# Kernel optimization log

Measured on AMD Instinct MI355X. Metric: run time of the kernel, lower is better.

## Reference

```python
import jax, jax.numpy as jnp
import numpy as np
from jax import lax

B, CIN, COUT, K, SDIM, H = 8, 512, 512, 3, 512, 32
EPS = 1e-8
LRELU_SLOPE = 0.2
ACT_SCALE = float(np.sqrt(2.0))


def setup_inputs() -> dict:
    key = jax.random.key(0)
    k1, k2, k3, k4 = jax.random.split(key, 4)
    return {
        "x": jax.random.normal(k1, (B, CIN, H, H), jnp.float32),
        "style": jax.random.normal(k2, (B, SDIM), jnp.float32),
        "weight": jax.random.normal(k3, (COUT, CIN, K, K), jnp.float32),
        "mod_w": jax.random.normal(k4, (CIN, SDIM), jnp.float32),
        "mod_b": jnp.ones((CIN,), jnp.float32),  # EqualLinear bias_init=1
        "bias": jnp.zeros((COUT,), jnp.float32),  # FusedLeakyReLU bias
    }


def _blur_kernel(c):
    bk = np.array([1.0, 3.0, 3.0, 1.0], np.float32)
    bk = bk[None, :] * bk[:, None]
    bk = bk / bk.sum() * 4.0  # upsample_factor ** 2
    return jnp.tile(jnp.asarray(bk)[None, None], (c, 1, 1, 1))  # (C,1,4,4)


def reference(x, style, weight, mod_w, mod_b, bias):
    b, cin, h, w = x.shape
    cout, k = weight.shape[0], weight.shape[-1]
    conv_scale = 1.0 / np.sqrt(cin * k * k)
    lin_scale = 1.0 / np.sqrt(mod_w.shape[1])

    # style modulation: EqualLinear(style_dim -> in_channel), bias_init=1
    s = style @ (mod_w * lin_scale).T + mod_b  # (B, Cin)

    # per-sample modulated weights (B, Cout, Cin, k, k)
    wmod = conv_scale * weight[None] * s[:, None, :, None, None]
    demod = lax.rsqrt(jnp.sum(wmod * wmod, axis=(2, 3, 4)) + EPS)
    wmod = wmod * demod[:, :, None, None, None]

    # conv_transpose2d(stride=2, pad=0) == conv with lhs_dilation=2, pad=k-1,
    # spatially-flipped kernel (torch transposes (Cout,Cin)->(Cin,Cout)).
    wflip = jnp.flip(wmod, (-2, -1))

    def convt(xi, wi):  # xi: (Cin,H,W), wi: (Cout,Cin,k,k)
        return lax.conv_general_dilated(
            xi[None], wi, (1, 1), [(k - 1, k - 1)] * 2,
            lhs_dilation=(2, 2),
            dimension_numbers=("NCHW", "OIHW", "NCHW"))[0]

    y = jax.vmap(convt)(x, wflip)  # (B, Cout, 2H+1, 2W+1)

    # Blur: upfirdn2d with pad=(1,1), depthwise 4x4 FIR (kernel symmetric)
    bk = _blur_kernel(cout)
    y = lax.conv_general_dilated(
        y, bk, (1, 1), [(1, 1), (1, 1)],
        feature_group_count=cout,
        dimension_numbers=("NCHW", "OIHW", "NCHW"))  # (B, Cout, 2H, 2W)

    # FusedLeakyReLU: leaky_relu(y + bias) * sqrt(2)
    z = y + bias[None, :, None, None]
    return jnp.where(z >= 0, z, LRELU_SLOPE * z) * ACT_SCALE
```

## Files before the change

kernel.cpp:

```cpp
#include <hip/hip_runtime.h>
#include <hip/hip_bf16.h>

#define NB 8
#define CIN 512
#define COUT 512
#define SDIM 512

typedef __attribute__((ext_vector_type(8))) short short8;
typedef __attribute__((ext_vector_type(4))) float f32x4;

static constexpr float CONV_SCALE = 0.014731391274719740f;
static constexpr float LIN_SCALE  = 0.044194173824159216f;

static constexpr size_t OFF_S     = 0;
static constexpr size_t OFF_WSQ   = 16384;
static constexpr size_t OFF_DEMOD = 1064960;
static constexpr size_t OFF_XP    = 1081344;
static constexpr size_t OFF_WP    = 10551296;
static constexpr size_t OFF_Y1    = 15269888;

static constexpr int NJOBS = 1060;

__device__ __forceinline__ int wpoff(int ps) {
  return ps == 0 ? 0 : ps == 1 ? 1048576 : ps == 2 ? 1572864 : 2097152;
}
__device__ __forceinline__ constexpr int PSPAD(int ps) {
  return ps == 0 ? 1090 : ps == 3 ? 1024 : 1056;
}
__device__ __forceinline__ constexpr int PLB(int ps) {
  return ps == 0 ? 0 : ps == 1 ? 4464640 : ps == 2 ? 8790016 : 13115392;
}

__device__ __forceinline__ short f2bf(float f) {
  unsigned u = __builtin_bit_cast(unsigned, f);
  unsigned r = (u + 0x7fffu + ((u >> 16) & 1u)) >> 16;
  return (short)r;
}
__device__ __forceinline__ float bf2f(unsigned short u) {
  return __builtin_bit_cast(float, (unsigned)u << 16);
}

__device__ __forceinline__ void load_lds16(const short* g, short* l) {
  __builtin_amdgcn_global_load_lds(
      (const __attribute__((address_space(1))) unsigned int*)g,
      (__attribute__((address_space(3))) unsigned int*)l, 16, 0, 0);
}

__global__ void k_prep1(const float* __restrict__ style, const float* __restrict__ mod_w,
                        const float* __restrict__ mod_b, float* __restrict__ s_out,
                        const float* __restrict__ w, short* __restrict__ wp,
                        float* __restrict__ wsq) {
  const int tid = threadIdx.x;
  if (blockIdx.x < 1024) {
    int idx = blockIdx.x * 256 + tid;
    int co = idx >> 9, ci = idx & 511;
    float wv[3][3];
    float sq = 0.f;
#pragma unroll
    for (int i = 0; i < 9; ++i) {
      float v = w[idx * 9 + i];
      wv[i / 3][i % 3] = v;
      sq += v * v;
    }
    wsq[idx] = sq * CONV_SCALE * CONV_SCALE;
#pragma unroll
    for (int wy = 0; wy < 3; ++wy)
#pragma unroll
      for (int wx = 0; wx < 3; ++wx) {
        int psy = (wy == 1) ? 1 : 0, psx = (wx == 1) ? 1 : 0;
        int u = psy ? 0 : (wy == 0 ? 1 : 0);
        int v = psx ? 0 : (wx == 0 ? 1 : 0);
        int ps = psy * 2 + psx;
        int tap = psy ? (psx ? 0 : v) : (psx ? u : u * 2 + v);
        int k = tap * 512 + ci;
        int elem = wpoff(ps) + ((k >> 6) * 512 + co) * 64 + (k & 63);
        wp[elem] = f2bf(wv[wy][wx] * CONV_SCALE);
      }
  } else {
    int wid = tid >> 6, lane = tid & 63;
    int ci = (blockIdx.x - 1024) * 4 + wid;
    float acc[NB] = {};
    for (int k = lane; k < SDIM; k += 64) {
      float wm = mod_w[ci * SDIM + k];
#pragma unroll
      for (int b = 0; b < NB; ++b) acc[b] += wm * style[b * SDIM + k];
    }
#pragma unroll
    for (int b = 0; b < NB; ++b) {
      float v = acc[b];
      for (int o = 32; o > 0; o >>= 1) v += __shfl_xor(v, o);
      if (lane == 0) s_out[b * CIN + ci] = v * LIN_SCALE + mod_b[ci];
    }
  }
}

__global__ void k_prep2(const float* __restrict__ wsq, const float* __restrict__ s,
                        float* __restrict__ demod,
                        const float* __restrict__ x, short* __restrict__ xp) {
  const int tid = threadIdx.x;
  if (blockIdx.x < 1024) {
    __shared__ float t[64][65];
    const int tx = tid & 63, ty = tid >> 6;
    int bx = blockIdx.x;
    int sp0 = (bx & 15) * 64, ci0 = ((bx >> 4) & 7) * 64, b = bx >> 7;
    for (int r = ty; r < 64; r += 4)
      t[r][tx] = x[(b * CIN + ci0 + r) * 1024 + sp0 + tx];
    __syncthreads();
    int ci = ci0 + tx;
    float sv = s[b * CIN + ci];
    for (int r = ty; r < 64; r += 4) {
      int sp = sp0 + r;
      int yy = sp >> 5, xx = sp & 31;
      xp[((b * 34 + yy + 1) * 34 + (xx + 1)) * 512 + ci] = f2bf(t[tx][r] * sv);
    }
  } else if (blockIdx.x < 1152) {
    int wid = tid >> 6, lane = tid & 63;
    int co = (blockIdx.x - 1024) * 4 + wid;
    float acc[NB] = {};
    for (int ci = lane; ci < CIN; ci += 64) {
      float wq = wsq[co * CIN + ci];
#pragma unroll
      for (int b = 0; b < NB; ++b) {
        float sv = s[b * CIN + ci];
        acc[b] += wq * sv * sv;
      }
    }
#pragma unroll
    for (int b = 0; b < NB; ++b) {
      float v = acc[b];
      for (int o = 32; o > 0; o >>= 1) v += __shfl_xor(v, o);
      if (lane == 0) demod[b * COUT + co] = rsqrtf(v + 1e-8f);
    }
  } else {
    int idx = blockIdx.x - 1152;
    int b = idx >> 2, part = idx & 3;
    unsigned* xpu = (unsigned*)xp;
    for (int k = 0; k < 33; ++k) {
      int c = part * 33 + k;
      int yy, xx;
      if (c < 34)       { yy = 0;            xx = c; }
      else if (c < 68)  { yy = 33;           xx = c - 34; }
      else if (c < 100) { yy = 1 + (c - 68); xx = 0; }
      else              { yy = 1 + (c - 100); xx = 33; }
      xpu[((((b * 34 + yy) * 34 + xx) * 512) >> 1) + tid] = 0u;
    }
  }
}

#define MFMA_ROWPAIR(AH, AL, RH, RL)                                              \
  __builtin_amdgcn_s_setprio(1);                                                  \
  acc[RH][0] = __builtin_amdgcn_mfma_f32_16x16x32_bf16(AH, b0, acc[RH][0], 0,0,0);\
  acc[RH][1] = __builtin_amdgcn_mfma_f32_16x16x32_bf16(AH, b1, acc[RH][1], 0,0,0);\
  acc[RH][2] = __builtin_amdgcn_mfma_f32_16x16x32_bf16(AH, b2, acc[RH][2], 0,0,0);\
  acc[RH][3] = __builtin_amdgcn_mfma_f32_16x16x32_bf16(AH, b3, acc[RH][3], 0,0,0);\
  acc[RL][0] = __builtin_amdgcn_mfma_f32_16x16x32_bf16(AL, b0, acc[RL][0], 0,0,0);\
  acc[RL][1] = __builtin_amdgcn_mfma_f32_16x16x32_bf16(AL, b1, acc[RL][1], 0,0,0);\
  acc[RL][2] = __builtin_amdgcn_mfma_f32_16x16x32_bf16(AL, b2, acc[RL][2], 0,0,0);\
  acc[RL][3] = __builtin_amdgcn_mfma_f32_16x16x32_bf16(AL, b3, acc[RL][3], 0,0,0);\
  __builtin_amdgcn_s_setprio(0);

__global__ __launch_bounds__(256, 2) void k_gemm(const short* __restrict__ xp,
                                                 const short* __restrict__ wp,
                                                 short* __restrict__ y1) {
  __shared__ short sW[2][128 * 64];
  __shared__ short sX[2][128 * 64];

  const int tid = threadIdx.x;
  const int wid = tid >> 6, lane = tid & 63;
  const int hi = lane >> 4;
  const int ksw8 = ((tid & 7) ^ ((tid >> 3) & 7)) * 8;
  const int wm = (wid >> 1) * 64, wn = (wid & 1) * 64;

  const int bx = blockIdx.x;
  const int xcd = bx & 7, ii = bx >> 3;
  const int j = (((ii >> 2) << 3) + xcd) * 4 + (ii & 3);
  if (j >= NJOBS) return;

  int ps, base;
  if (j < 276)      { ps = 0; base = 0; }
  else if (j < 540) { ps = 1; base = 276; }
  else if (j < 804) { ps = 2; base = 540; }
  else              { ps = 3; base = 804; }
  const int r = j - base;
  const int nb = r >> 2, mb = r & 3;
  const int psy = ps >> 1, psx = ps & 1;
  const int Ny = 33 - psy, Nx = 33 - psx;
  const int NyNx = Ny * Nx;
  const int N = NB * NyNx;
  const int n0 = nb * 128, m0 = mb * 128;
  const int KT = (2 - psy) * (2 - psx) * 8;
  const short* wpb = wp + wpoff(ps);

  int bb[4], ay[4], ax[4];
#pragma unroll
  for (int i = 0; i < 4; ++i) {
    int seg = i * 256 + tid;
    int n = n0 + (seg >> 3);
    if (n >= N) n = N - 1;
    int b = n / NyNx;
    int rem = n - b * NyNx;
    int a_y = rem / Nx;
    bb[i] = b; ay[i] = a_y; ax[i] = rem - a_y * Nx;
  }

  auto STAGE = [&](int kt, int d) {
    int tap = kt >> 3, ci0 = (kt & 7) << 6;
    int oy, ox;
    if (ps == 0)      { oy = tap >> 1; ox = tap & 1; }
    else if (ps == 1) { oy = tap;      ox = 1; }
    else if (ps == 2) { oy = 1;        ox = tap; }
    else              { oy = 1;        ox = 1; }
#pragma unroll
    for (int i = 0; i < 4; ++i) {
      int seg = i * 256 + tid;
      const short* gw = wpb + (kt * 512 + m0 + (seg >> 3)) * 64 + ksw8;
      load_lds16(gw, &sW[d][(i * 4 + wid) * 512]);
    }
#pragma unroll
    for (int i = 0; i < 4; ++i) {
      const short* gx = xp + ((bb[i] * 34 + ay[i] + oy) * 34 + ax[i] + ox) * 512 + ci0 + ksw8;
      load_lds16(gx, &sX[d][(i * 4 + wid) * 512]);
    }
  };

  const int c0 = ((hi)     ^ (lane & 7)) * 8;
  const int c1 = ((4 + hi) ^ (lane & 7)) * 8;
  const int rA0 = (wm +  0 + (lane & 15)) * 64, rA1 = (wm + 16 + (lane & 15)) * 64;
  const int rA2 = (wm + 32 + (lane & 15)) * 64, rA3 = (wm + 48 + (lane & 15)) * 64;
  const int rB0 = (wn +  0 + (lane & 15)) * 64, rB1 = (wn + 16 + (lane & 15)) * 64;
  const int rB2 = (wn + 32 + (lane & 15)) * 64, rB3 = (wn + 48 + (lane & 15)) * 64;

  f32x4 acc[4][4] = {};

  STAGE(0, 0);
  STAGE(1, 1);
  __syncthreads();

  int cur = 0;
  for (int t = 0; t < KT; ++t) {
    const short* W = sW[cur];
    const short* X = sX[cur];
    short8 a0, a1, b0, b1, b2, b3;

    a0 = *(const short8*)&W[rA0 + c0];
    a1 = *(const short8*)&W[rA1 + c0];
    b0 = *(const short8*)&X[rB0 + c0];
    b1 = *(const short8*)&X[rB1 + c0];
    b2 = *(const short8*)&X[rB2 + c0];
    b3 = *(const short8*)&X[rB3 + c0];
    MFMA_ROWPAIR(a0, a1, 0, 1);
    __builtin_amdgcn_s_barrier();

    a0 = *(const short8*)&W[rA2 + c0];
    a1 = *(const short8*)&W[rA3 + c0];
    MFMA_ROWPAIR(a0, a1, 2, 3);
    __builtin_amdgcn_s_barrier();

    a0 = *(const short8*)&W[rA0 + c1];
    a1 = *(const short8*)&W[rA1 + c1];
    b0 = *(const short8*)&X[rB0 + c1];
    b1 = *(const short8*)&X[rB1 + c1];
    b2 = *(const short8*)&X[rB2 + c1];
    b3 = *(const short8*)&X[rB3 + c1];
    MFMA_ROWPAIR(a0, a1, 0, 1);
    __builtin_amdgcn_s_barrier();

    a0 = *(const short8*)&W[rA2 + c1];
    a1 = *(const short8*)&W[rA3 + c1];
    MFMA_ROWPAIR(a0, a1, 2, 3);

    __syncthreads();
    if (t + 2 < KT) STAGE(t + 2, cur);
    cur ^= 1;
  }

  const int psp = PSPAD(ps);
  const int plb = PLB(ps);
#pragma unroll
  for (int nf = 0; nf < 4; ++nf) {
    int n = n0 + wn + nf * 16 + (lane & 15);
    if (n < N) {
      int b = n / NyNx;
      int rem = n - b * NyNx;
      int nbase = plb + b * psp + rem;
#pragma unroll
      for (int mf = 0; mf < 4; ++mf) {
        int m = m0 + wm + mf * 16 + (lane >> 4) * 4;
#pragma unroll
        for (int rr = 0; rr < 4; ++rr)
          y1[nbase + (m + rr) * 8 * psp] = f2bf(acc[mf][nf][rr]);
      }
    }
  }
}

__global__ __launch_bounds__(256, 8) void k_blur(const short* __restrict__ y1,
                                                 const float* __restrict__ demod,
                                                 const float* __restrict__ bias,
                                                 float* __restrict__ out) {
  __shared__ float sin_[4][18 * 35];
  __shared__ float stmp[2][18][64];
  const int tid = threadIdx.x;
  const int bc = blockIdx.x & 4095;
  const int h = blockIdx.x >> 12;
  const int co = bc & 511, b = bc >> 9;
  const int m0v = h * 16;

  for (int i = tid; i < 4 * 18 * 35; i += 256) ((float*)sin_)[i] = 0.f;
  __syncthreads();

#pragma unroll
  for (int ps = 0; ps < 4; ++ps) {
    const int Nyv = 33 - (ps >> 1), Nxv = 33 - (ps & 1);
    const int total = Nyv * Nxv;
    const short* pl = y1 + PLB(ps) + (co * NB + b) * PSPAD(ps);
    for (int t2 = tid; t2 * 2 < total; t2 += 256) {
      int e0 = t2 * 2;
      unsigned pair = *(const unsigned*)&pl[e0];
      int av0 = e0 / Nxv, ah0 = e0 - av0 * Nxv;
      int lr0 = av0 + 1 - m0v;
      if (lr0 >= 0 && lr0 < 18)
        sin_[ps][lr0 * 35 + ah0 + 1] = bf2f((unsigned short)(pair & 0xffffu));
      int e1 = e0 + 1;
      if (e1 < total) {
        int av1 = e1 / Nxv, ah1 = e1 - av1 * Nxv;
        int lr1 = av1 + 1 - m0v;
        if (lr1 >= 0 && lr1 < 18)
          sin_[ps][lr1 * 35 + ah1 + 1] = bf2f((unsigned short)(pair >> 16));
      }
    }
  }
  __syncthreads();

  const int q = tid & 63;
  const int mx = q >> 1, fx = q & 1;
  int xp0, xi0, xp1, xi1, xp2, xi2, xp3, xi3;
  if (fx) { xp0 = 0; xi0 = mx + 1; xp1 = 1; xi1 = mx + 1; xp2 = 0; xi2 = mx + 2; xp3 = 1; xi3 = mx + 2; }
  else    { xp0 = 1; xi0 = mx;     xp1 = 0; xi1 = mx + 1; xp2 = 1; xi2 = mx + 1; xp3 = 0; xi3 = mx + 2; }

  for (int rt = tid >> 6; rt < 36; rt += 4) {
    int pv = (rt >= 18) ? 1 : 0;
    int lr = rt - pv * 18;
    if (m0v + lr < 35) {
      float v = 0.25f * sin_[pv * 2 + xp0][lr * 35 + xi0]
              + 0.75f * sin_[pv * 2 + xp1][lr * 35 + xi1]
              + 0.75f * sin_[pv * 2 + xp2][lr * 35 + xi2]
              + 0.25f * sin_[pv * 2 + xp3][lr * 35 + xi3];
      stmp[pv][lr][q] = v;
    } else {
      stmp[pv][lr][q] = 0.f;
    }
  }
  __syncthreads();

  const float dm = demod[b * COUT + co], bs = bias[co];
  for (int pl_ = tid >> 6; pl_ < 32; pl_ += 4) {
    int myl = pl_ >> 1, fy = pl_ & 1;
    float v;
    if (fy) v = 0.25f * stmp[0][myl + 1][q] + 0.75f * stmp[1][myl + 1][q]
              + 0.75f * stmp[0][myl + 2][q] + 0.25f * stmp[1][myl + 2][q];
    else    v = 0.25f * stmp[1][myl][q]     + 0.75f * stmp[0][myl + 1][q]
              + 0.75f * stmp[1][myl + 1][q] + 0.25f * stmp[0][myl + 2][q];
    float val = dm * v + bs;
    int p = h * 32 + pl_;
    out[(bc * 64 + p) * 64 + q] = (val >= 0.f ? val : 0.2f * val) * 1.41421356237309515f;
  }
}

extern "C" void kernel_launch(void* const* d_in, const int* in_sizes, int n_in,
                              void* d_out, int out_size, void* d_ws, size_t ws_size,
                              hipStream_t stream) {
  const float* x      = (const float*)d_in[0];
  const float* style  = (const float*)d_in[1];
  const float* weight = (const float*)d_in[2];
  const float* mod_w  = (const float*)d_in[3];
  const float* mod_b  = (const float*)d_in[4];
  const float* bias   = (const float*)d_in[5];
  float* out = (float*)d_out;
  char* ws = (char*)d_ws;

  float* s     = (float*)(ws + OFF_S);
  float* wsq   = (float*)(ws + OFF_WSQ);
  float* demod = (float*)(ws + OFF_DEMOD);
  short* xp    = (short*)(ws + OFF_XP);
  short* wp    = (short*)(ws + OFF_WP);
  short* y1    = (short*)(ws + OFF_Y1);

  k_prep1<<<1152, 256, 0, stream>>>(style, mod_w, mod_b, s, weight, wp, wsq);
  k_prep2<<<1184, 256, 0, stream>>>(wsq, s, demod, x, xp);
  k_gemm<<<1088, 256, 0, stream>>>(xp, wp, y1);
  k_blur<<<8192, 256, 0, stream>>>(y1, demod, bias, out);
}
```

Baseline: 117.1 us.

## Load modulated weight fragments directly to registers, drop weight LDS staging

The GEMM kernel no longer stages weight tiles through shared memory. Each wave loads its A-operand fragments straight from global memory into registers, double-buffered across k-steps, while only the activation tile stays in LDS. Halving LDS use allows raising the occupancy hint from 2 to 3 blocks per CU, and the intra-iteration barriers are removed. The cost is more registers for the weight fragments and uncoalesced, latency-exposed global loads.

```diff
diff --git a/kernel.cpp b/kernel.cpp
--- a/kernel.cpp
+++ b/kernel.cpp
@@ -147,22 +147,9 @@
   }
 }
 
-#define MFMA_ROWPAIR(AH, AL, RH, RL)                                              \
-  __builtin_amdgcn_s_setprio(1);                                                  \
-  acc[RH][0] = __builtin_amdgcn_mfma_f32_16x16x32_bf16(AH, b0, acc[RH][0], 0,0,0);\
-  acc[RH][1] = __builtin_amdgcn_mfma_f32_16x16x32_bf16(AH, b1, acc[RH][1], 0,0,0);\
-  acc[RH][2] = __builtin_amdgcn_mfma_f32_16x16x32_bf16(AH, b2, acc[RH][2], 0,0,0);\
-  acc[RH][3] = __builtin_amdgcn_mfma_f32_16x16x32_bf16(AH, b3, acc[RH][3], 0,0,0);\
-  acc[RL][0] = __builtin_amdgcn_mfma_f32_16x16x32_bf16(AL, b0, acc[RL][0], 0,0,0);\
-  acc[RL][1] = __builtin_amdgcn_mfma_f32_16x16x32_bf16(AL, b1, acc[RL][1], 0,0,0);\
-  acc[RL][2] = __builtin_amdgcn_mfma_f32_16x16x32_bf16(AL, b2, acc[RL][2], 0,0,0);\
-  acc[RL][3] = __builtin_amdgcn_mfma_f32_16x16x32_bf16(AL, b3, acc[RL][3], 0,0,0);\
-  __builtin_amdgcn_s_setprio(0);
-
-__global__ __launch_bounds__(256, 2) void k_gemm(const short* __restrict__ xp,
+__global__ __launch_bounds__(256, 3) void k_gemm(const short* __restrict__ xp,
                                                  const short* __restrict__ wp,
                                                  short* __restrict__ y1) {
-  __shared__ short sW[2][128 * 64];
   __shared__ short sX[2][128 * 64];
 
   const int tid = threadIdx.x;
@@ -202,76 +189,76 @@
     int a_y = rem / Nx;
     bb[i] = b; ay[i] = a_y; ax[i] = rem - a_y * Nx;
   }
-
-  auto STAGE = [&](int kt, int d) {
+  const short* xbase[4];
+#pragma unroll
+  for (int i = 0; i < 4; ++i)
+    xbase[i] = xp + ((bb[i] * 34 + ay[i]) * 34 + ax[i]) * 512 + ksw8;
+
+  auto STAGEX = [&](int kt, int d) {
     int tap = kt >> 3, ci0 = (kt & 7) << 6;
     int oy, ox;
     if (ps == 0)      { oy = tap >> 1; ox = tap & 1; }
     else if (ps == 1) { oy = tap;      ox = 1; }
     else if (ps == 2) { oy = 1;        ox = tap; }
     else              { oy = 1;        ox = 1; }
-#pragma unroll
-    for (int i = 0; i < 4; ++i) {
-      int seg = i * 256 + tid;
-      const short* gw = wpb + (kt * 512 + m0 + (seg >> 3)) * 64 + ksw8;
-      load_lds16(gw, &sW[d][(i * 4 + wid) * 512]);
-    }
-#pragma unroll
-    for (int i = 0; i < 4; ++i) {
-      const short* gx = xp + ((bb[i] * 34 + ay[i] + oy) * 34 + ax[i] + ox) * 512 + ci0 + ksw8;
-      load_lds16(gx, &sX[d][(i * 4 + wid) * 512]);
-    }
+    int goff = (oy * 34 + ox) * 512 + ci0;
+#pragma unroll
+    for (int i = 0; i < 4; ++i)
+      load_lds16(xbase[i] + goff, &sX[d][(i * 4 + wid) * 512]);
+  };
+
+  const short* wbase[4];
+#pragma unroll
+  for (int mf = 0; mf < 4; ++mf)
+    wbase[mf] = wpb + (m0 + wm + mf * 16 + (lane & 15)) * 64 + hi * 8;
+
+  short8 wA[4][2], wB[4][2];
+  auto LOADW = [&](int kt, short8 (&Wf)[4][2]) {
+#pragma unroll
+    for (int mf = 0; mf < 4; ++mf)
+#pragma unroll
+      for (int ks = 0; ks < 2; ++ks)
+        Wf[mf][ks] = *(const short8*)(wbase[mf] + kt * 32768 + ks * 32);
   };
 
   const int c0 = ((hi)     ^ (lane & 7)) * 8;
   const int c1 = ((4 + hi) ^ (lane & 7)) * 8;
-  const int rA0 = (wm +  0 + (lane & 15)) * 64, rA1 = (wm + 16 + (lane & 15)) * 64;
-  const int rA2 = (wm + 32 + (lane & 15)) * 64, rA3 = (wm + 48 + (lane & 15)) * 64;
-  const int rB0 = (wn +  0 + (lane & 15)) * 64, rB1 = (wn + 16 + (lane & 15)) * 64;
-  const int rB2 = (wn + 32 + (lane & 15)) * 64, rB3 = (wn + 48 + (lane & 15)) * 64;
+  int rB[4];
+#pragma unroll
+  for (int nf = 0; nf < 4; ++nf) rB[nf] = (wn + nf * 16 + (lane & 15)) * 64;
 
   f32x4 acc[4][4] = {};
 
-  STAGE(0, 0);
-  STAGE(1, 1);
+  auto COMPUTE = [&](const short* X, short8 (&Wf)[4][2]) {
+#pragma unroll
+    for (int ks = 0; ks < 2; ++ks) {
+      short8 bf[4];
+#pragma unroll
+      for (int nf = 0; nf < 4; ++nf)
+        bf[nf] = *(const short8*)&X[rB[nf] + (ks ? c1 : c0)];
+      __builtin_amdgcn_s_setprio(1);
+#pragma unroll
+      for (int mf = 0; mf < 4; ++mf)
+#pragma unroll
+        for (int nf = 0; nf < 4; ++nf)
+          acc[mf][nf] = __builtin_amdgcn_mfma_f32_16x16x32_bf16(Wf[mf][ks], bf[nf], acc[mf][nf], 0, 0, 0);
+      __builtin_amdgcn_s_setprio(0);
+    }
+  };
+
+  STAGEX(0, 0);
+  STAGEX(1, 1);
+  LOADW(0, wA);
   __syncthreads();
 
-  int cur = 0;
-  for (int t = 0; t < KT; ++t) {
-    const short* W = sW[cur];
-    const short* X = sX[cur];
-    short8 a0, a1, b0, b1, b2, b3;
-
-    a0 = *(const short8*)&W[rA0 + c0];
-    a1 = *(const short8*)&W[rA1 + c0];
-    b0 = *(const short8*)&X[rB0 + c0];
-    b1 = *(const short8*)&X[rB1 + c0];
-    b2 = *(const short8*)&X[rB2 + c0];
-    b3 = *(const short8*)&X[rB3 + c0];
-    MFMA_ROWPAIR(a0, a1, 0, 1);
-    __builtin_amdgcn_s_barrier();
-
-    a0 = *(const short8*)&W[rA2 + c0];
-    a1 = *(const short8*)&W[rA3 + c0];
-    MFMA_ROWPAIR(a0, a1, 2, 3);
-    __builtin_amdgcn_s_barrier();
-
-    a0 = *(const short8*)&W[rA0 + c1];
-    a1 = *(const short8*)&W[rA1 + c1];
-    b0 = *(const short8*)&X[rB0 + c1];
-    b1 = *(const short8*)&X[rB1 + c1];
-    b2 = *(const short8*)&X[rB2 + c1];
-    b3 = *(const short8*)&X[rB3 + c1];
-    MFMA_ROWPAIR(a0, a1, 0, 1);
-    __builtin_amdgcn_s_barrier();
-
-    a0 = *(const short8*)&W[rA2 + c1];
-    a1 = *(const short8*)&W[rA3 + c1];
-    MFMA_ROWPAIR(a0, a1, 2, 3);
-
+  for (int tt = 0; tt < KT; tt += 2) {
+    LOADW(tt + 1, wB);
+    COMPUTE(sX[0], wA);
     __syncthreads();
-    if (t + 2 < KT) STAGE(t + 2, cur);
-    cur ^= 1;
+    if (tt + 2 < KT) { STAGEX(tt + 2, 0); LOADW(tt + 2, wA); }
+    COMPUTE(sX[1], wB);
+    __syncthreads();
+    if (tt + 3 < KT) STAGEX(tt + 3, 1);
   }
 
   const int psp = PSPAD(ps);
```

Measured after the change: 196.5 us. 1.68x slower.
